# Kernel optimization log

Hardware: AMD Instinct MI355X
Metric: run time of the kernel (lower is better)

The kernel has to match this reference:

```python
import jax, jax.numpy as jnp
import numpy as np

B, L, V = 16, 2048, 64


def setup_inputs() -> dict:
    key = jax.random.key(0)
    k1, k2, k3, k4 = jax.random.split(key, 4)
    idx = jax.random.randint(k1, (B, L), 0, V)                      # tokens
    Wq_w = jax.random.normal(k2, (V, V), jnp.float32) * 0.02         # nn.Linear weight
    Wv_w = jax.random.normal(k3, (V, V), jnp.float32) * 0.02 + np.float32(np.e)  # Wv.weight (+e init)
    v_emb = jax.random.normal(k4, (L, 1), jnp.float32) * 0.02        # nn.Embedding(length, 1)
    return {"idx": idx, "Wq_w": Wq_w, "Wv_w": Wv_w, "v_emb": v_emb}


def reference(idx, Wq_w, Wv_w, v_emb):
    Lx = v_emb.shape[0]
    Vx = Wq_w.shape[0]
    # e = one_hot token embedding, [B, L, V]
    e = jax.nn.one_hot(idx, Vx, dtype=jnp.float32)
    i = jnp.arange(Lx)
    # pos[i, j] = max(i - j, 0); learned relative-position score table [L, L]
    pos = jnp.maximum(i[:, None] - i[None, :], 0)
    pos_embd = v_emb[pos, 0]
    causal = i[:, None] >= i[None, :]                                # tril mask
    # Attention block 1: scores are the learned position table (no QK^T)
    attn1 = jax.nn.softmax(jnp.where(causal, pos_embd, -jnp.inf), axis=-1)  # [L, L]
    l1 = jnp.einsum('ts,bsv->btv', attn1, e)                         # [B, L, V]
    # Attention block 2: Wq(e) @ l1^T, masked softmax, attn @ e * scalar
    q = jnp.einsum('btv,uv->btu', e, Wq_w)                           # F.linear: e @ Wq^T
    scores = jnp.einsum('btv,bsv->bts', q, l1)                       # [B, L, L]
    attn2 = jax.nn.softmax(jnp.where(causal, scores, -jnp.inf), axis=-1)
    l2 = jnp.einsum('bts,bsv->btv', attn2, e) * Wv_w[0, 0]           # logits [B, L, V]
    return l2
```

## Files before the change

kernel.cpp:

```cpp
#include <hip/hip_runtime.h>


#define LSEQ 2048
#define NB 16
#define NV 64
#define NC 32

typedef __attribute__((ext_vector_type(8))) short bf16x8;
typedef __attribute__((ext_vector_type(4))) float f32x4;

__device__ __forceinline__ unsigned short f2bf(float f) {
  unsigned int u = __float_as_uint(f);
  return (unsigned short)((u + 0x7FFFu + ((u >> 16) & 1u)) >> 16);
}

__global__ __launch_bounds__(256) void k_gather(const int* __restrict__ idx,
                                                const float* __restrict__ Wq,
                                                const float* __restrict__ v_emb,
                                                unsigned short* __restrict__ Agr,
                                                unsigned short* __restrict__ Ebf,
                                                float* __restrict__ S) {
  const int b = blockIdx.x >> 4;
  const int tile = blockIdx.x & 15;
  const int w = threadIdx.x >> 6;
  const int lane = threadIdx.x & 63;

  if (blockIdx.x == 0 && threadIdx.x < 64) {
    const int base = lane * 32;
    float e[32];
    float run = 0.f;
#pragma unroll
    for (int i = 0; i < 32; ++i) { e[i] = expf(v_emb[base + i]); run += e[i]; }
    float incl = run;
#pragma unroll
    for (int d = 1; d < 64; d <<= 1) {
      float up = __shfl_up(incl, d);
      if (lane >= d) incl += up;
    }
    float acc = incl - run;
#pragma unroll
    for (int i = 0; i < 32; ++i) {
      acc += e[i];
      Ebf[base + i] = f2bf(e[i]);
      S[base + i] = acc;
    }
  }

  const int k8base = tile * 16 + w * 4;
#pragma unroll
  for (int r = 0; r < 4; ++r) {
    const int k8 = k8base + r;
    unsigned short v[8];
#pragma unroll
    for (int j = 0; j < 8; ++j) {
      const int ii = idx[b * LSEQ + (2047 - (k8 * 8 + j))];
      v[j] = f2bf(Wq[ii * 64 + lane]);
    }
    uint4 st;
    st.x = (unsigned int)v[0] | ((unsigned int)v[1] << 16);
    st.y = (unsigned int)v[2] | ((unsigned int)v[3] << 16);
    st.z = (unsigned int)v[4] | ((unsigned int)v[5] << 16);
    st.w = (unsigned int)v[6] | ((unsigned int)v[7] << 16);
    *(uint4*)(Agr + ((size_t)(b * 256 + k8) * 64 + lane) * 8) = st;
  }
}

__global__ __launch_bounds__(256) void k_gemm(const unsigned short* __restrict__ Agr,
                                              const unsigned short* __restrict__ Ebf,
                                              const float* __restrict__ S,
                                              float* __restrict__ P) {
  __shared__ unsigned short GL0[2208];
  __shared__ unsigned short GL1[2176];
  __shared__ float red[16][64];
  __shared__ float red2[16][64];

  const int b  = blockIdx.y;
  const int bn = 63 - (int)blockIdx.x;
  const int n0 = bn * 32;
  const int tid = threadIdx.x;
  const int w = tid >> 6;
  const int lane = tid & 63;
  const int quad = lane >> 4;
  const int lm = lane & 15;
  const int nsub = w & 1;
  const int kh = w >> 1;

  {
    const int wend = n0 + 160;
    for (int i = 96 + tid; i < wend; i += 256) {
      const int e0 = i - 127;
      const int e1 = i - 126;
      GL0[i] = (e0 >= 0 && e0 < LSEQ) ? Ebf[e0] : (unsigned short)0;
      GL1[i] = (e1 >= 0 && e1 < LSEQ) ? Ebf[e1] : (unsigned short)0;
    }
  }
  __syncthreads();

  f32x4 acc[4];
#pragma unroll
  for (int mt = 0; mt < 4; ++mt) acc[mt] = (f32x4){0.f, 0.f, 0.f, 0.f};

  const int nbase = n0 + nsub * 16;
  const int sbase = nbase + lm - 1920;
  const int kstart = 2048 - (n0 + 32);
  const int iters = bn + 1;
  const unsigned short* __restrict__ abase = Agr + (size_t)b * 256 * 64 * 8;

  union AF { uint4 u; bf16x8 v; };
  union BF { unsigned int u[4]; bf16x8 v; };
  AF a[3][4];
  BF bb[3];

#define LOAD_FRAGS(J_, SL) do {                                             \
    const int k_ = kstart + (kh + 2 * (J_)) * 32;                           \
    const int kq8_ = (k_ >> 3) + quad;                                      \
    const unsigned short* ab_ = abase + ((size_t)kq8_ * 64 + lm) * 8;       \
    a[SL][0].u = *(const uint4*)(ab_ + 0 * 128);                            \
    a[SL][1].u = *(const uint4*)(ab_ + 1 * 128);                            \
    a[SL][2].u = *(const uint4*)(ab_ + 2 * 128);                            \
    a[SL][3].u = *(const uint4*)(ab_ + 3 * 128);                            \
    const int s_ = sbase + k_ + quad * 8;                                   \
    const unsigned int* gb_ = (s_ & 1) ? (const unsigned int*)GL1           \
                                       : (const unsigned int*)GL0;          \
    const int off_ = s_ >> 1;                                               \
    bb[SL].u[0] = gb_[off_ + 0]; bb[SL].u[1] = gb_[off_ + 1];               \
    bb[SL].u[2] = gb_[off_ + 2]; bb[SL].u[3] = gb_[off_ + 3];               \
  } while (0)

#define MFMA4(SL) do {                                                      \
    acc[0] = __builtin_amdgcn_mfma_f32_16x16x32_bf16(a[SL][0].v, bb[SL].v, acc[0], 0, 0, 0); \
    acc[1] = __builtin_amdgcn_mfma_f32_16x16x32_bf16(a[SL][1].v, bb[SL].v, acc[1], 0, 0, 0); \
    acc[2] = __builtin_amdgcn_mfma_f32_16x16x32_bf16(a[SL][2].v, bb[SL].v, acc[2], 0, 0, 0); \
    acc[3] = __builtin_amdgcn_mfma_f32_16x16x32_bf16(a[SL][3].v, bb[SL].v, acc[3], 0, 0, 0); \
  } while (0)

  const int J = (iters > kh) ? ((iters - kh + 1) >> 1) : 0;
  if (J > 0) {
    LOAD_FRAGS(0, 0);
    if (J > 1) LOAD_FRAGS(1, 1);
    int j = 0;
    while (true) {
      if (j + 2 < J) LOAD_FRAGS(j + 2, 2);
      MFMA4(0);
      if (++j >= J) break;
      if (j + 2 < J) LOAD_FRAGS(j + 2, 0);
      MFMA4(1);
      if (++j >= J) break;
      if (j + 2 < J) LOAD_FRAGS(j + 2, 1);
      MFMA4(2);
      if (++j >= J) break;
    }
  }
#undef LOAD_FRAGS
#undef MFMA4

  if (kh == 1) {
    float (*rd)[64] = nsub ? red2 : red;
#pragma unroll
    for (int mt = 0; mt < 4; ++mt)
#pragma unroll
      for (int r = 0; r < 4; ++r) rd[mt * 4 + r][lane] = acc[mt][r];
  }
  __syncthreads();
  if (kh == 0) {
    float (*rd)[64] = nsub ? red2 : red;
#pragma unroll
    for (int mt = 0; mt < 4; ++mt)
#pragma unroll
      for (int r = 0; r < 4; ++r) acc[mt][r] += rd[mt * 4 + r][lane];

    const float sinv = 1.0f / S[nbase + lm];
#pragma unroll
    for (int mt = 0; mt < 4; ++mt) {
#pragma unroll
      for (int r = 0; r < 4; ++r) {
        const int c = mt * 16 + quad * 4 + r;
        P[((size_t)(b * 64 + c)) * LSEQ + nbase + lm] = __expf(acc[mt][r] * sinv);
      }
    }
  }
}

__global__ __launch_bounds__(256) void k_hist2(const int* __restrict__ idx,
                                               const float* __restrict__ P,
                                               float* __restrict__ hist) {
  __shared__ float Hs[NC][65];
  const int bc = blockIdx.x;
  const int b = bc >> 6;
  const int w = threadIdx.x >> 6;
  const int lane = threadIdx.x & 63;

  for (int i = threadIdx.x; i < NC * 65; i += 256) ((float*)Hs)[i] = 0.f;
  __syncthreads();

  const float* __restrict__ prow = P + (size_t)bc * LSEQ;
  const int* __restrict__ irow = idx + b * LSEQ;
  float p[8]; int ii[8];
#pragma unroll
  for (int r = 0; r < 8; ++r) {
    const int ch = w * 8 + r;
    p[r] = prow[ch * 64 + lane];
    ii[r] = irow[ch * 64 + lane];
  }
#pragma unroll
  for (int r = 0; r < 8; ++r) atomicAdd(&Hs[w * 8 + r][ii[r]], p[r]);
  __syncthreads();

  const int half = lane >> 5, l32 = lane & 31;
#pragma unroll
  for (int r = 0; r < 8; ++r) {
    const int v = w * 16 + r * 2 + half;
    const float h = Hs[l32][v];
    float x = h;
#pragma unroll
    for (int d = 1; d < 32; d <<= 1) {
      float up = __shfl_up(x, d, 32);
      if (l32 >= d) x += up;
    }
    Hs[l32][v] = x - h;
  }
  __syncthreads();

  float* __restrict__ hrow = hist + (size_t)bc * NC * 64;
#pragma unroll
  for (int r = 0; r < 8; ++r) {
    const int ch = w * 8 + r;
    hrow[ch * 64 + lane] = Hs[ch][lane];
  }
}

__global__ __launch_bounds__(256) void k_emit(const int* __restrict__ idx,
                                              const float* __restrict__ P,
                                              const float* __restrict__ hist,
                                              const float* __restrict__ Wv,
                                              float* __restrict__ out) {
  __shared__ float bins[4][64];
  const int tg = blockIdx.x;
  const int b  = blockIdx.y;
  const int w = threadIdx.x >> 6;
  const int lane = threadIdx.x & 63;
  const int t = tg * 4 + w;
  const int c = idx[b * LSEQ + t];
  const int bc = b * 64 + c;
  const int ch = t >> 6;
  const int rel = t & 63;

  float p = P[(size_t)bc * LSEQ + ch * 64 + lane];
  const int ii = idx[b * LSEQ + ch * 64 + lane];
  const float he = hist[((size_t)bc * NC + ch) * 64 + lane];
  p = (lane <= rel) ? p : 0.f;
  bins[w][lane] = 0.f;
  __threadfence_block();
  atomicAdd(&bins[w][ii], p);
  __threadfence_block();
  const float bin = bins[w][lane] + he;

  float z = bin;
#pragma unroll
  for (int d = 1; d < 64; d <<= 1) z += __shfl_xor(z, d);
  out[((size_t)(b * LSEQ + t)) * 64 + lane] = Wv[0] * bin / z;
}

extern "C" void kernel_launch(void* const* d_in, const int* in_sizes, int n_in,
                              void* d_out, int out_size, void* d_ws, size_t ws_size,
                              hipStream_t stream) {
  const int* idx     = (const int*)d_in[0];
  const float* Wq    = (const float*)d_in[1];
  const float* Wv    = (const float*)d_in[2];
  const float* v_emb = (const float*)d_in[3];
  float* out = (float*)d_out;

  float* S = (float*)d_ws;
  float* P = S + LSEQ;
  float* hist = P + (size_t)NB * NV * LSEQ;
  unsigned short* Ebf = (unsigned short*)(hist + (size_t)NB * NV * NC * 64);
  unsigned short* Agr = Ebf + LSEQ;

  k_gather<<<NB * 16, 256, 0, stream>>>(idx, Wq, v_emb, Agr, Ebf, S);
  k_gemm<<<dim3(64, NB), 256, 0, stream>>>(Agr, Ebf, S, P);
  k_hist2<<<NB * NV, 256, 0, stream>>>(idx, P, hist);
  k_emit<<<dim3(LSEQ / 4, NB), 256, 0, stream>>>(idx, P, hist, Wv, out);
}
```

Measured before the change: 120.8 us.

## Fuse histogram prefix scan and output emission into one kernel

Merges the per-(batch,token-class) chunk histogram scan kernel with the emit kernel. Each block now loops over the positions whose token equals its class, found by ballot, and writes output rows straight from the shared-memory prefix histogram. This removes the global hist buffer write and read and one kernel launch. In exchange, per-block work becomes uneven because it depends on how many tokens match the class, and the per-position loop is serial within each wave.

```diff
diff --git a/kernel.cpp b/kernel.cpp
--- a/kernel.cpp
+++ b/kernel.cpp
@@ -181,20 +181,21 @@
   }
 }
 
-__global__ __launch_bounds__(256) void k_hist2(const int* __restrict__ idx,
-                                               const float* __restrict__ P,
-                                               float* __restrict__ hist) {
+__global__ __launch_bounds__(256) void k_scanemit(const int* __restrict__ idx,
+                                                  const float* __restrict__ P,
+                                                  const float* __restrict__ Wv,
+                                                  float* __restrict__ out) {
   __shared__ float Hs[NC][65];
+  __shared__ float bins[4][64];
   const int bc = blockIdx.x;
   const int b = bc >> 6;
+  const int c = bc & 63;
   const int w = threadIdx.x >> 6;
   const int lane = threadIdx.x & 63;
 
-  for (int i = threadIdx.x; i < NC * 65; i += 256) ((float*)Hs)[i] = 0.f;
-  __syncthreads();
-
   const float* __restrict__ prow = P + (size_t)bc * LSEQ;
   const int* __restrict__ irow = idx + b * LSEQ;
+
   float p[8]; int ii[8];
 #pragma unroll
   for (int r = 0; r < 8; ++r) {
@@ -202,6 +203,8 @@
     p[r] = prow[ch * 64 + lane];
     ii[r] = irow[ch * 64 + lane];
   }
+  for (int i = threadIdx.x; i < NC * 65; i += 256) ((float*)Hs)[i] = 0.f;
+  __syncthreads();
 #pragma unroll
   for (int r = 0; r < 8; ++r) atomicAdd(&Hs[w * 8 + r][ii[r]], p[r]);
   __syncthreads();
@@ -221,44 +224,27 @@
   }
   __syncthreads();
 
-  float* __restrict__ hrow = hist + (size_t)bc * NC * 64;
+  const float wv = Wv[0];
 #pragma unroll
   for (int r = 0; r < 8; ++r) {
     const int ch = w * 8 + r;
-    hrow[ch * 64 + lane] = Hs[ch][lane];
-  }
-}
-
-__global__ __launch_bounds__(256) void k_emit(const int* __restrict__ idx,
-                                              const float* __restrict__ P,
-                                              const float* __restrict__ hist,
-                                              const float* __restrict__ Wv,
-                                              float* __restrict__ out) {
-  __shared__ float bins[4][64];
-  const int tg = blockIdx.x;
-  const int b  = blockIdx.y;
-  const int w = threadIdx.x >> 6;
-  const int lane = threadIdx.x & 63;
-  const int t = tg * 4 + w;
-  const int c = idx[b * LSEQ + t];
-  const int bc = b * 64 + c;
-  const int ch = t >> 6;
-  const int rel = t & 63;
-
-  float p = P[(size_t)bc * LSEQ + ch * 64 + lane];
-  const int ii = idx[b * LSEQ + ch * 64 + lane];
-  const float he = hist[((size_t)bc * NC + ch) * 64 + lane];
-  p = (lane <= rel) ? p : 0.f;
-  bins[w][lane] = 0.f;
-  __threadfence_block();
-  atomicAdd(&bins[w][ii], p);
-  __threadfence_block();
-  const float bin = bins[w][lane] + he;
-
-  float z = bin;
-#pragma unroll
-  for (int d = 1; d < 64; d <<= 1) z += __shfl_xor(z, d);
-  out[((size_t)(b * LSEQ + t)) * 64 + lane] = Wv[0] * bin / z;
+    unsigned long long m = __ballot(ii[r] == c);
+    while (m) {
+      const int srel = __builtin_ctzll(m);
+      m &= m - 1;
+      const int t = ch * 64 + srel;
+      const float pm = (lane <= srel) ? p[r] : 0.f;
+      bins[w][lane] = 0.f;
+      __threadfence_block();
+      atomicAdd(&bins[w][ii[r]], pm);
+      __threadfence_block();
+      const float bin = bins[w][lane] + Hs[ch][lane];
+      float z = bin;
+#pragma unroll
+      for (int d = 1; d < 64; d <<= 1) z += __shfl_xor(z, d);
+      out[((size_t)(b * LSEQ + t)) * 64 + lane] = wv * bin / z;
+    }
+  }
 }
 
 extern "C" void kernel_launch(void* const* d_in, const int* in_sizes, int n_in,
@@ -272,12 +258,10 @@
 
   float* S = (float*)d_ws;
   float* P = S + LSEQ;
-  float* hist = P + (size_t)NB * NV * LSEQ;
-  unsigned short* Ebf = (unsigned short*)(hist + (size_t)NB * NV * NC * 64);
+  unsigned short* Ebf = (unsigned short*)(P + (size_t)NB * NV * LSEQ);
   unsigned short* Agr = Ebf + LSEQ;
 
   k_gather<<<NB * 16, 256, 0, stream>>>(idx, Wq, v_emb, Agr, Ebf, S);
   k_gemm<<<dim3(64, NB), 256, 0, stream>>>(Agr, Ebf, S, P);
-  k_hist2<<<NB * NV, 256, 0, stream>>>(idx, P, hist);
-  k_emit<<<dim3(LSEQ / 4, NB), 256, 0, stream>>>(idx, P, hist, Wv, out);
-}
+  k_scanemit<<<NB * NV, 256, 0, stream>>>(idx, P, Wv, out);
+}
```

New measurement: 120.3 us, median of 2. About the same (-0.4%).
